# Optimization experiments

Hardware: AMD Instinct MI355X
Metric: run time of the kernel (lower is better)

The kernel has to match this reference:

```python
import jax, jax.numpy as jnp
import numpy as np

NUME = 100000
H, DH, K, R = 4, 32, 16, 17
DIN, DT, DOUT = 128, 32, 128
N0, N1, N2 = 131072, 32768, 4096
B, HIST = 2048, 2
LN_EPS = 1e-5


def setup_inputs() -> dict:
    key = jax.random.key(0)
    ks = jax.random.split(key, 16)
    din = DIN + DT
    inp = {}
    inp["emb"] = jax.random.normal(ks[0], (NUME, DIN), jnp.float32) * 0.1
    inp["freq"] = jnp.asarray(1.0 / 10 ** np.linspace(0, 9, DT), jnp.float32)
    inp["phase"] = jnp.zeros((DT,), jnp.float32)
    for l in (0, 1):
        inp[f"gamma{l}"] = jnp.ones((din,), jnp.float32)
        inp[f"beta{l}"] = jnp.zeros((din,), jnp.float32)
        inp[f"W{l}"] = jax.random.normal(ks[1 + 5 * l], (R, din, H * DH), jnp.float32) * 0.05
        inp[f"attn_l{l}"] = jax.random.normal(ks[2 + 5 * l], (R, H, DH), jnp.float32) * 0.05
        inp[f"attn_r{l}"] = jax.random.normal(ks[3 + 5 * l], (R, H, DH), jnp.float32) * 0.05
        inp[f"bias{l}"] = jnp.zeros((R, H * DH), jnp.float32)
    inp["src_ids0"] = jax.random.randint(ks[11], (N0,), 0, NUME * 100)
    inp["src_idx0"] = jax.random.randint(ks[12], (R, N1, K), 0, N0)
    inp["src_ids1"] = jax.random.randint(ks[13], (N1,), 0, NUME * 100)
    inp["src_idx1"] = jax.random.randint(ks[14], (R, N2, K), 0, N1)
    inp["root_idx"] = jax.random.randint(ks[15], (B * HIST,), 0, N2)
    inp["ts"] = 99
    return inp


def _gat_layer(h, src_ids, src_idx, gamma, beta, W, al, ar, b, ts, freq, phase):
    # h: [Nsrc, din-DT] src-node features; src_idx: [R, Ndst, K] neighbor ids.
    ndst = src_idx.shape[1]
    # TimeEnc: cos((ts - nid // nume) * freq + phase)
    t = (ts - src_ids // NUME).astype(h.dtype)
    phi = jnp.cos(t[:, None] * freq + phase)  # [Nsrc, DT]
    h = jnp.concatenate([h, phi], axis=1)
    # LayerNorm
    mu = jnp.mean(h, axis=-1, keepdims=True)
    var = jnp.mean((h - mu) ** 2, axis=-1, keepdims=True)
    h = (h - mu) * jax.lax.rsqrt(var + LN_EPS) * gamma + beta

    def body(acc, xs):
        Wr, alr, arr, br, idx = xs
        proj = (h @ Wr).reshape(-1, H, DH)               # [Nsrc, H, DH]
        el = jnp.einsum('nhe,he->nh', proj, alr)         # [Nsrc, H]
        er = jnp.einsum('nhe,he->nh', proj[:ndst], arr)  # [Ndst, H]
        e = jax.nn.leaky_relu(el[idx] + er[:, None, :], 0.2)  # [Ndst, K, H]
        a = jax.nn.softmax(e, axis=1)                    # edge softmax over K
        out = jnp.einsum('ikh,ikhe->ihe', a, proj[idx]) + br.reshape(H, DH)
        return acc + out, None

    acc, _ = jax.lax.scan(body, jnp.zeros((ndst, H, DH), h.dtype),
                          (W, al, ar, b, src_idx))
    # HeteroGraphConv aggregate='mean' over R relation outputs, then ReLU
    return jax.nn.relu((acc / R).reshape(ndst, H * DH))


def reference(emb, freq, phase,
              gamma0, beta0, W0, attn_l0, attn_r0, bias0,
              gamma1, beta1, W1, attn_l1, attn_r1, bias1,
              src_ids0, src_idx0, src_ids1, src_idx1, root_idx, ts):
    h = emb[src_ids0 % NUME]  # entity embedding lookup [N0, DIN]
    h = _gat_layer(h, src_ids0, src_idx0, gamma0, beta0, W0, attn_l0, attn_r0,
                   bias0, ts, freq, phase)
    h = _gat_layer(h, src_ids1, src_idx1, gamma1, beta1, W1, attn_l1, attn_r1,
                   bias1, ts, freq, phase)
    # gather root embeddings and fold hist dimension into features
    return h[root_idx].reshape(B, HIST * DOUT)
```

## Files before the change

kernel.cpp:

```cpp
#include <hip/hip_runtime.h>
#include <hip/hip_bf16.h>

#define NUME 100000
constexpr int H      = 4;
constexpr int DH     = 32;
constexpr int KNB    = 16;
constexpr int R      = 17;
constexpr int DIN    = 128;
constexpr int DT     = 32;
constexpr int DINT   = 160;
constexpr int N0     = 131072;
constexpr int N1     = 32768;
constexpr int N2     = 4096;
constexpr float LN_EPS = 1e-5f;

typedef unsigned short ushort_t;
typedef ushort_t us2 __attribute__((ext_vector_type(2)));
typedef ushort_t us8 __attribute__((ext_vector_type(8)));
typedef short    s8v __attribute__((ext_vector_type(8)));
typedef float    f32x4 __attribute__((ext_vector_type(4)));

__device__ __forceinline__ float bf2f(ushort_t u) {
    return __uint_as_float(((unsigned int)u) << 16);
}
__device__ __forceinline__ ushort_t f2bf(float f) {
    unsigned int x = __float_as_uint(f);
    unsigned int r = x + 0x7fffu + ((x >> 16) & 1u);
    return (ushort_t)(r >> 16);
}

__global__ __launch_bounds__(256) void k_wcast(
    const float* __restrict__ W, ushort_t* __restrict__ wt, int total)
{
    int t = blockIdx.x * blockDim.x + threadIdx.x;
    if (t >= total) return;
    int r   = t / (DINT * DIN);
    int rem = t % (DINT * DIN);
    int k   = rem >> 7;
    int n   = rem & 127;
    wt[(size_t)r * DIN * DINT + (size_t)n * DINT + k] = f2bf(W[t]);
}

__global__ __launch_bounds__(256) void k_prep(
    const float* __restrict__ srcf,
    const int*   __restrict__ ids,
    const int*   __restrict__ ts_ptr,
    const float* __restrict__ freq,
    const float* __restrict__ phase,
    const float* __restrict__ gamma,
    const float* __restrict__ beta,
    ushort_t*    __restrict__ hn,
    int n_rows, int mode)
{
    int wid  = (int)((blockIdx.x * blockDim.x + threadIdx.x) >> 6);
    int lane = threadIdx.x & 63;
    if (wid >= n_rows) return;

    int id = ids[wid];
    const float* row = (mode == 1)
        ? (srcf + (size_t)(id % NUME) * DIN)
        : (srcf + (size_t)wid * DIN);

    float x0 = row[lane];
    float x1 = row[lane + 64];
    if (mode == 0) {
        x0 = fmaxf(x0 * (1.f / (float)R), 0.f);
        x1 = fmaxf(x1 * (1.f / (float)R), 0.f);
    }

    int   ts = ts_ptr[0];
    float t  = (float)(ts - id / NUME);
    float p  = 0.f;
    if (lane < DT) p = cosf(t * freq[lane] + phase[lane]);

    float s  = x0 + x1 + p;
    float sq = x0*x0 + x1*x1 + p*p;
    #pragma unroll
    for (int m = 1; m < 64; m <<= 1) {
        s  += __shfl_xor(s,  m);
        sq += __shfl_xor(sq, m);
    }
    float mu   = s / (float)DINT;
    float var  = sq / (float)DINT - mu * mu;
    float rstd = rsqrtf(var + LN_EPS);

    size_t base = (size_t)wid * DINT;
    hn[base + lane]      = f2bf((x0 - mu) * rstd * gamma[lane]      + beta[lane]);
    hn[base + 64 + lane] = f2bf((x1 - mu) * rstd * gamma[64 + lane] + beta[64 + lane]);
    if (lane < DT)
        hn[base + 128 + lane] = f2bf((p - mu) * rstd * gamma[128 + lane] + beta[128 + lane]);
}

__global__ __launch_bounds__(256) void k_gemm(
    const ushort_t* __restrict__ A,
    const ushort_t* __restrict__ Bt,
    const float*    __restrict__ al,
    const float*    __restrict__ ar,
    ushort_t*       __restrict__ C,
    float*          __restrict__ el,
    float*          __restrict__ er,
    int ndst)
{
    __shared__ ushort_t Bs[128][168];
    __shared__ ushort_t As[2][128][40];

    int tid  = threadIdx.x;
    int lane = tid & 63;
    int wave = tid >> 6;
    int wr   = wave >> 1;
    int wc   = wave & 1;
    int row0 = blockIdx.x * 128;

    {
        int bm  = tid >> 1;
        int bko = (tid & 1) * 80;
        #pragma unroll
        for (int g = 0; g < 10; ++g)
            *(us8*)&Bs[bm][bko + g * 8] =
                *(const us8*)&Bt[(size_t)bm * DINT + bko + g * 8];
        #pragma unroll
        for (int j = 0; j < 2; ++j) {
            int f  = tid + j * 256;
            int m  = f >> 2;
            int ko = (f & 3) * 8;
            *(us8*)&As[0][m][ko] = *(const us8*)&A[(size_t)(row0 + m) * DINT + ko];
        }
    }
    __syncthreads();

    s8v breg[5][4];
    #pragma unroll
    for (int kk = 0; kk < 5; ++kk)
        #pragma unroll
        for (int j = 0; j < 4; ++j)
            breg[kk][j] = *(const s8v*)&Bs[wc*64 + j*16 + (lane & 15)]
                                          [kk*32 + (lane >> 4) * 8];

    f32x4 acc[4][4];
    #pragma unroll
    for (int i = 0; i < 4; ++i)
        #pragma unroll
        for (int j = 0; j < 4; ++j) acc[i][j] = (f32x4){0.f, 0.f, 0.f, 0.f};

    #pragma unroll
    for (int kc = 0; kc < 5; ++kc) {
        us8 pa[2];
        int m0 = 0, ko0 = 0, m1 = 0, ko1 = 0;
        if (kc < 4) {
            int f0 = tid;
            m0  = f0 >> 2; ko0 = (f0 & 3) * 8;
            pa[0] = *(const us8*)&A[(size_t)(row0 + m0) * DINT + (kc + 1) * 32 + ko0];
            int f1 = tid + 256;
            m1  = f1 >> 2; ko1 = (f1 & 3) * 8;
            pa[1] = *(const us8*)&A[(size_t)(row0 + m1) * DINT + (kc + 1) * 32 + ko1];
        }

        s8v af[4];
        #pragma unroll
        for (int i = 0; i < 4; ++i)
            af[i] = *(const s8v*)&As[kc & 1][wr*64 + i*16 + (lane & 15)]
                                            [(lane >> 4) * 8];
        #pragma unroll
        for (int i = 0; i < 4; ++i)
            #pragma unroll
            for (int j = 0; j < 4; ++j)
                acc[i][j] = __builtin_amdgcn_mfma_f32_16x16x32_bf16(
                                af[i], breg[kc][j], acc[i][j], 0, 0, 0);

        if (kc < 4) {
            *(us8*)&As[(kc + 1) & 1][m0][ko0] = pa[0];
            *(us8*)&As[(kc + 1) & 1][m1][ko1] = pa[1];
        }
        __syncthreads();
    }

    #pragma unroll
    for (int i = 0; i < 4; ++i) {
        #pragma unroll
        for (int j = 0; j < 4; ++j) {
            int col  = wc*64 + j*16 + (lane & 15);
            int rowb = row0 + wr*64 + i*16 + ((lane >> 4) << 2);
            #pragma unroll
            for (int q = 0; q < 4; ++q)
                C[(size_t)(rowb + q) * DIN + col] = f2bf(acc[i][j][q]);
        }
    }

    float alv[4], arv[4];
    #pragma unroll
    for (int j = 0; j < 4; ++j) {
        int c = wc*64 + j*16 + (lane & 15);
        alv[j] = al[c];
        arv[j] = ar[c];
    }
    int b0 = lane & 1;
    int b1 = (lane >> 1) & 1;
    #pragma unroll
    for (int i = 0; i < 4; ++i) {
        #pragma unroll
        for (int q = 0; q < 4; ++q) {
            float pl0 = acc[i][0][q]*alv[0] + acc[i][1][q]*alv[1];
            float pl1 = acc[i][2][q]*alv[2] + acc[i][3][q]*alv[3];
            float pr0 = acc[i][0][q]*arv[0] + acc[i][1][q]*arv[1];
            float pr1 = acc[i][2][q]*arv[2] + acc[i][3][q]*arv[3];
            float t;
            t = __shfl_xor(b0 ? pl0 : pl1, 1);
            float vA = (b0 ? pl1 : pl0) + t;
            t = __shfl_xor(b0 ? pr0 : pr1, 1);
            float vB = (b0 ? pr1 : pr0) + t;
            t = __shfl_xor(b1 ? vA : vB, 2);
            float vC = (b1 ? vB : vA) + t;
            vC += __shfl_xor(vC, 4);
            vC += __shfl_xor(vC, 8);
            if ((lane & 12) == 0) {
                int row = row0 + wr*64 + i*16 + ((lane >> 4) << 2) + q;
                int h   = 2*wc + b0;
                if (!b1) {
                    el[(size_t)row * 4 + h] = vC;
                } else if (row < ndst) {
                    er[(size_t)row * 4 + h] = vC;
                }
            }
        }
    }
}

__global__ __launch_bounds__(256) void k_agg(
    const ushort_t* __restrict__ proj,
    const int*      __restrict__ idx,
    const float*    __restrict__ el,
    const float*    __restrict__ er,
    const float*    __restrict__ br,
    float*          __restrict__ accg,
    int ndst)
{
    int wid  = (int)((blockIdx.x * blockDim.x + threadIdx.x) >> 6);
    if (wid >= ndst) return;
    int l = threadIdx.x & 63;

    int jv = idx[(size_t)wid * KNB + (l & 15)];

    int   jk = __shfl(jv, l >> 2);
    float e  = el[(size_t)jk * 4 + (l & 3)] + er[(size_t)wid * 4 + (l & 3)];
    e = e > 0.f ? e : 0.2f * e;
    float mx = e;
    #pragma unroll
    for (int m = 4; m < 64; m <<= 1) mx = fmaxf(mx, __shfl_xor(mx, m));
    float p = __expf(e - mx);
    float s = p;
    #pragma unroll
    for (int m = 4; m < 64; m <<= 1) s += __shfl_xor(s, m);
    float a = p / s;

    int rsub = l >> 4;
    int fg   = l & 15;
    float vacc[8];
    #pragma unroll
    for (int t = 0; t < 8; ++t) vacc[t] = 0.f;

    #pragma unroll
    for (int kk = 0; kk < 4; ++kk) {
        int   j  = __shfl(jv, 4*kk + rsub);
        float ak = __shfl(a, 16*kk + 4*rsub + (fg >> 2));
        us8   v  = *(const us8*)&proj[(size_t)j * DIN + fg * 8];
        #pragma unroll
        for (int t = 0; t < 8; ++t) vacc[t] = fmaf(ak, bf2f(v[t]), vacc[t]);
    }
    #pragma unroll
    for (int t = 0; t < 8; ++t) {
        vacc[t] += __shfl_xor(vacc[t], 16);
        vacc[t] += __shfl_xor(vacc[t], 32);
    }
    if (l < 16) {
        float* ap = accg + (size_t)wid * DIN + l * 8;
        #pragma unroll
        for (int t = 0; t < 8; ++t) ap[t] += vacc[t] + br[l * 8 + t];
    }
}

__global__ __launch_bounds__(256) void k_root(
    const float* __restrict__ acc, const int* __restrict__ root,
    float* __restrict__ out, int n)
{
    int t = blockIdx.x * blockDim.x + threadIdx.x;
    if (t < n) {
        float x = acc[(size_t)root[t >> 7] * DIN + (t & 127)];
        out[t] = fmaxf(x * (1.f / (float)R), 0.f);
    }
}

extern "C" void kernel_launch(void* const* d_in, const int* in_sizes, int n_in,
                              void* d_out, int out_size, void* d_ws, size_t ws_size,
                              hipStream_t stream)
{
    const float* emb    = (const float*)d_in[0];
    const float* freq   = (const float*)d_in[1];
    const float* phase  = (const float*)d_in[2];
    const float* gamma0 = (const float*)d_in[3];
    const float* beta0  = (const float*)d_in[4];
    const float* W0     = (const float*)d_in[5];
    const float* al0    = (const float*)d_in[6];
    const float* ar0    = (const float*)d_in[7];
    const float* b0     = (const float*)d_in[8];
    const float* gamma1 = (const float*)d_in[9];
    const float* beta1  = (const float*)d_in[10];
    const float* W1     = (const float*)d_in[11];
    const float* al1    = (const float*)d_in[12];
    const float* ar1    = (const float*)d_in[13];
    const float* b1     = (const float*)d_in[14];
    const int* src_ids0 = (const int*)d_in[15];
    const int* src_idx0 = (const int*)d_in[16];
    const int* src_ids1 = (const int*)d_in[17];
    const int* src_idx1 = (const int*)d_in[18];
    const int* root     = (const int*)d_in[19];
    const int* ts       = (const int*)d_in[20];
    float* out = (float*)d_out;

    ushort_t* hn   = (ushort_t*)d_ws;
    ushort_t* proj = hn   + (size_t)N0 * DINT;
    float*    acc  = (float*)(proj + (size_t)N0 * DIN);
    float*    el   = acc  + (size_t)N1 * DIN;
    float*    er   = el   + (size_t)N0 * 4;
    ushort_t* wt0  = (ushort_t*)(er + (size_t)N1 * 4);
    ushort_t* wt1  = wt0 + (size_t)R * DIN * DINT;

    const int WTOT = R * DINT * DIN;

    k_wcast<<<(WTOT + 255) / 256, 256, 0, stream>>>(W0, wt0, WTOT);
    hipMemsetAsync(acc, 0, (size_t)N1 * DIN * sizeof(float), stream);
    k_prep<<<N0 / 4, 256, 0, stream>>>(emb, src_ids0, ts, freq, phase,
                                       gamma0, beta0, hn, N0, 1);
    for (int r = 0; r < R; ++r) {
        k_gemm<<<N0 / 128, 256, 0, stream>>>(hn, wt0 + (size_t)r * DIN * DINT,
                                             al0 + r * 128, ar0 + r * 128,
                                             proj, el, er, N1);
        k_agg<<<N1 / 4, 256, 0, stream>>>(proj,
                                          src_idx0 + (size_t)r * N1 * KNB,
                                          el, er, b0 + r * 128, acc, N1);
    }

    k_wcast<<<(WTOT + 255) / 256, 256, 0, stream>>>(W1, wt1, WTOT);
    k_prep<<<N1 / 4, 256, 0, stream>>>(acc, src_ids1, ts, freq, phase,
                                       gamma1, beta1, hn, N1, 0);
    hipMemsetAsync(acc, 0, (size_t)N2 * DIN * sizeof(float), stream);
    for (int r = 0; r < R; ++r) {
        k_gemm<<<N1 / 128, 256, 0, stream>>>(hn, wt1 + (size_t)r * DIN * DINT,
                                             al1 + r * 128, ar1 + r * 128,
                                             proj, el, er, N2);
        k_agg<<<N2 / 4, 256, 0, stream>>>(proj,
                                          src_idx1 + (size_t)r * N2 * KNB,
                                          el, er, b1 + r * 128, acc, N2);
    }

    k_root<<<(N2 * DIN) / 256, 256, 0, stream>>>(acc, root, out, N2 * DIN);
}
```

Baseline: 1.447 ms.

## Batch layer-1 relations into one GEMM and fused aggregation, hoist bias sums

Layer 1 now runs one GEMM launch over all 17 relations via blockIdx.y, storing per-relation projections, followed by a single aggregation kernel. That kernel loops over relations in registers and writes acc once, which removes 34 launches and the repeated read-modify-write of acc. Per-relation biases are pre-summed once and folded into the next prep step or the root kernel instead of being added on every aggregation. Prep handles two rows per wave with float4 loads, and the aggregation kernel issues its neighbor loads before the softmax to hide latency. The batched path needs extra workspace and falls back to the old loop when ws_size is too small.

Measured after the change: 1.208 ms. -16.6%, faster.

```diff
diff --git a/kernel.cpp b/kernel.cpp
--- a/kernel.cpp
+++ b/kernel.cpp
@@ -15,7 +15,7 @@
 constexpr float LN_EPS = 1e-5f;
 
 typedef unsigned short ushort_t;
-typedef ushort_t us2 __attribute__((ext_vector_type(2)));
+typedef ushort_t us4 __attribute__((ext_vector_type(4)));
 typedef ushort_t us8 __attribute__((ext_vector_type(8)));
 typedef short    s8v __attribute__((ext_vector_type(8)));
 typedef float    f32x4 __attribute__((ext_vector_type(4)));
@@ -39,6 +39,19 @@
     int k   = rem >> 7;
     int n   = rem & 127;
     wt[(size_t)r * DIN * DINT + (size_t)n * DINT + k] = f2bf(W[t]);
+}
+
+__global__ __launch_bounds__(256) void k_bsum(
+    const float* __restrict__ b0, const float* __restrict__ b1,
+    float* __restrict__ bsum01)
+{
+    int t = threadIdx.x;
+    const float* b = (t < 128) ? b0 : b1;
+    int c = t & 127;
+    float s = 0.f;
+    #pragma unroll
+    for (int r = 0; r < R; ++r) s += b[r * 128 + c];
+    bsum01[t] = s;
 }
 
 __global__ __launch_bounds__(256) void k_prep(
@@ -49,34 +62,39 @@
     const float* __restrict__ phase,
     const float* __restrict__ gamma,
     const float* __restrict__ beta,
+    const float* __restrict__ bsum,
     ushort_t*    __restrict__ hn,
     int n_rows, int mode)
 {
-    int wid  = (int)((blockIdx.x * blockDim.x + threadIdx.x) >> 6);
+    int wv   = (int)((blockIdx.x * blockDim.x + threadIdx.x) >> 6);
     int lane = threadIdx.x & 63;
-    if (wid >= n_rows) return;
-
-    int id = ids[wid];
-    const float* row = (mode == 1)
+    int half = lane >> 5;
+    int l5   = lane & 31;
+    int row  = wv * 2 + half;
+    if (row >= n_rows) return;
+
+    int id = ids[row];
+    const float* rp = (mode == 1)
         ? (srcf + (size_t)(id % NUME) * DIN)
-        : (srcf + (size_t)wid * DIN);
-
-    float x0 = row[lane];
-    float x1 = row[lane + 64];
+        : (srcf + (size_t)row * DIN);
+
+    float4 x = *(const float4*)&rp[l5 * 4];
     if (mode == 0) {
-        x0 = fmaxf(x0 * (1.f / (float)R), 0.f);
-        x1 = fmaxf(x1 * (1.f / (float)R), 0.f);
+        const float4 bs = *(const float4*)&bsum[l5 * 4];
+        x.x = fmaxf((x.x + bs.x) * (1.f / (float)R), 0.f);
+        x.y = fmaxf((x.y + bs.y) * (1.f / (float)R), 0.f);
+        x.z = fmaxf((x.z + bs.z) * (1.f / (float)R), 0.f);
+        x.w = fmaxf((x.w + bs.w) * (1.f / (float)R), 0.f);
     }
 
     int   ts = ts_ptr[0];
     float t  = (float)(ts - id / NUME);
-    float p  = 0.f;
-    if (lane < DT) p = cosf(t * freq[lane] + phase[lane]);
-
-    float s  = x0 + x1 + p;
-    float sq = x0*x0 + x1*x1 + p*p;
-    #pragma unroll
-    for (int m = 1; m < 64; m <<= 1) {
+    float p  = cosf(t * freq[l5] + phase[l5]);
+
+    float s  = x.x + x.y + x.z + x.w + p;
+    float sq = x.x*x.x + x.y*x.y + x.z*x.z + x.w*x.w + p*p;
+    #pragma unroll
+    for (int m = 1; m < 32; m <<= 1) {
         s  += __shfl_xor(s,  m);
         sq += __shfl_xor(sq, m);
     }
@@ -84,25 +102,36 @@
     float var  = sq / (float)DINT - mu * mu;
     float rstd = rsqrtf(var + LN_EPS);
 
-    size_t base = (size_t)wid * DINT;
-    hn[base + lane]      = f2bf((x0 - mu) * rstd * gamma[lane]      + beta[lane]);
-    hn[base + 64 + lane] = f2bf((x1 - mu) * rstd * gamma[64 + lane] + beta[64 + lane]);
-    if (lane < DT)
-        hn[base + 128 + lane] = f2bf((p - mu) * rstd * gamma[128 + lane] + beta[128 + lane]);
+    size_t base = (size_t)row * DINT;
+    us4 pk;
+    pk[0] = f2bf((x.x - mu) * rstd * gamma[l5*4+0] + beta[l5*4+0]);
+    pk[1] = f2bf((x.y - mu) * rstd * gamma[l5*4+1] + beta[l5*4+1]);
+    pk[2] = f2bf((x.z - mu) * rstd * gamma[l5*4+2] + beta[l5*4+2]);
+    pk[3] = f2bf((x.w - mu) * rstd * gamma[l5*4+3] + beta[l5*4+3]);
+    *(us4*)&hn[base + l5*4] = pk;
+    hn[base + 128 + l5] = f2bf((p - mu) * rstd * gamma[128 + l5] + beta[128 + l5]);
 }
 
 __global__ __launch_bounds__(256) void k_gemm(
     const ushort_t* __restrict__ A,
-    const ushort_t* __restrict__ Bt,
-    const float*    __restrict__ al,
-    const float*    __restrict__ ar,
-    ushort_t*       __restrict__ C,
-    float*          __restrict__ el,
-    float*          __restrict__ er,
-    int ndst)
+    const ushort_t* __restrict__ BtB,
+    const float*    __restrict__ alB,
+    const float*    __restrict__ arB,
+    ushort_t*       __restrict__ CB,
+    float*          __restrict__ elB,
+    float*          __restrict__ erB,
+    int ndst, int M)
 {
     __shared__ ushort_t Bs[128][168];
     __shared__ ushort_t As[2][128][40];
+
+    int r = blockIdx.y;
+    const ushort_t* Bt = BtB + (size_t)r * DIN * DINT;
+    const float*    al = alB + (size_t)r * DIN;
+    const float*    ar = arB + (size_t)r * DIN;
+    ushort_t*       C  = CB  + (size_t)r * M * DIN;
+    float*          el = elB + (size_t)r * M * 4;
+    float*          er = erB + (size_t)r * ndst * 4;
 
     int tid  = threadIdx.x;
     int lane = tid & 63;
@@ -225,20 +254,29 @@
     }
 }
 
-__global__ __launch_bounds__(256) void k_agg(
+__global__ __launch_bounds__(256) void k_agg_r(
     const ushort_t* __restrict__ proj,
     const int*      __restrict__ idx,
     const float*    __restrict__ el,
     const float*    __restrict__ er,
-    const float*    __restrict__ br,
     float*          __restrict__ accg,
     int ndst)
 {
     int wid  = (int)((blockIdx.x * blockDim.x + threadIdx.x) >> 6);
     if (wid >= ndst) return;
-    int l = threadIdx.x & 63;
+    int l    = threadIdx.x & 63;
+    int rsub = l >> 4;
+    int fg   = l & 15;
 
     int jv = idx[(size_t)wid * KNB + (l & 15)];
+
+    int j2[4];
+    us8 v[4];
+    #pragma unroll
+    for (int kk = 0; kk < 4; ++kk) j2[kk] = __shfl(jv, 4*kk + rsub);
+    #pragma unroll
+    for (int kk = 0; kk < 4; ++kk)
+        v[kk] = *(const us8*)&proj[(size_t)j2[kk] * DIN + fg * 8];
 
     int   jk = __shfl(jv, l >> 2);
     float e  = el[(size_t)jk * 4 + (l & 3)] + er[(size_t)wid * 4 + (l & 3)];
@@ -252,19 +290,14 @@
     for (int m = 4; m < 64; m <<= 1) s += __shfl_xor(s, m);
     float a = p / s;
 
-    int rsub = l >> 4;
-    int fg   = l & 15;
     float vacc[8];
     #pragma unroll
     for (int t = 0; t < 8; ++t) vacc[t] = 0.f;
-
     #pragma unroll
     for (int kk = 0; kk < 4; ++kk) {
-        int   j  = __shfl(jv, 4*kk + rsub);
         float ak = __shfl(a, 16*kk + 4*rsub + (fg >> 2));
-        us8   v  = *(const us8*)&proj[(size_t)j * DIN + fg * 8];
-        #pragma unroll
-        for (int t = 0; t < 8; ++t) vacc[t] = fmaf(ak, bf2f(v[t]), vacc[t]);
+        #pragma unroll
+        for (int t = 0; t < 8; ++t) vacc[t] = fmaf(ak, bf2f(v[kk][t]), vacc[t]);
     }
     #pragma unroll
     for (int t = 0; t < 8; ++t) {
@@ -274,17 +307,83 @@
     if (l < 16) {
         float* ap = accg + (size_t)wid * DIN + l * 8;
         #pragma unroll
-        for (int t = 0; t < 8; ++t) ap[t] += vacc[t] + br[l * 8 + t];
+        for (int t = 0; t < 8; ++t) ap[t] += vacc[t];
+    }
+}
+
+__global__ __launch_bounds__(256) void k_agg_all(
+    const ushort_t* __restrict__ projB,
+    const int*      __restrict__ idxB,
+    const float*    __restrict__ elB,
+    const float*    __restrict__ erB,
+    float*          __restrict__ accg,
+    int ndst, int nsrc)
+{
+    int wid  = (int)((blockIdx.x * blockDim.x + threadIdx.x) >> 6);
+    if (wid >= ndst) return;
+    int l    = threadIdx.x & 63;
+    int rsub = l >> 4;
+    int fg   = l & 15;
+
+    float vacc[8];
+    #pragma unroll
+    for (int t = 0; t < 8; ++t) vacc[t] = 0.f;
+
+    for (int r = 0; r < R; ++r) {
+        const ushort_t* proj = projB + (size_t)r * nsrc * DIN;
+        const int*      idx  = idxB  + (size_t)r * ndst * KNB;
+        const float*    el   = elB   + (size_t)r * nsrc * 4;
+        const float*    er   = erB   + (size_t)r * ndst * 4;
+
+        int jv = idx[(size_t)wid * KNB + (l & 15)];
+
+        int j2[4];
+        us8 v[4];
+        #pragma unroll
+        for (int kk = 0; kk < 4; ++kk) j2[kk] = __shfl(jv, 4*kk + rsub);
+        #pragma unroll
+        for (int kk = 0; kk < 4; ++kk)
+            v[kk] = *(const us8*)&proj[(size_t)j2[kk] * DIN + fg * 8];
+
+        int   jk = __shfl(jv, l >> 2);
+        float e  = el[(size_t)jk * 4 + (l & 3)] + er[(size_t)wid * 4 + (l & 3)];
+        e = e > 0.f ? e : 0.2f * e;
+        float mx = e;
+        #pragma unroll
+        for (int m = 4; m < 64; m <<= 1) mx = fmaxf(mx, __shfl_xor(mx, m));
+        float p = __expf(e - mx);
+        float s = p;
+        #pragma unroll
+        for (int m = 4; m < 64; m <<= 1) s += __shfl_xor(s, m);
+        float a = p / s;
+
+        #pragma unroll
+        for (int kk = 0; kk < 4; ++kk) {
+            float ak = __shfl(a, 16*kk + 4*rsub + (fg >> 2));
+            #pragma unroll
+            for (int t = 0; t < 8; ++t) vacc[t] = fmaf(ak, bf2f(v[kk][t]), vacc[t]);
+        }
+    }
+
+    #pragma unroll
+    for (int t = 0; t < 8; ++t) {
+        vacc[t] += __shfl_xor(vacc[t], 16);
+        vacc[t] += __shfl_xor(vacc[t], 32);
+    }
+    if (l < 16) {
+        float* ap = accg + (size_t)wid * DIN + l * 8;
+        #pragma unroll
+        for (int t = 0; t < 8; ++t) ap[t] = vacc[t];
     }
 }
 
 __global__ __launch_bounds__(256) void k_root(
     const float* __restrict__ acc, const int* __restrict__ root,
-    float* __restrict__ out, int n)
+    const float* __restrict__ bsum1, float* __restrict__ out, int n)
 {
     int t = blockIdx.x * blockDim.x + threadIdx.x;
     if (t < n) {
-        float x = acc[(size_t)root[t >> 7] * DIN + (t & 127)];
+        float x = acc[(size_t)root[t >> 7] * DIN + (t & 127)] + bsum1[t & 127];
         out[t] = fmaxf(x * (1.f / (float)R), 0.f);
     }
 }
@@ -316,41 +415,62 @@
     const int* ts       = (const int*)d_in[20];
     float* out = (float*)d_out;
 
-    ushort_t* hn   = (ushort_t*)d_ws;
-    ushort_t* proj = hn   + (size_t)N0 * DINT;
-    float*    acc  = (float*)(proj + (size_t)N0 * DIN);
-    float*    el   = acc  + (size_t)N1 * DIN;
-    float*    er   = el   + (size_t)N0 * 4;
-    ushort_t* wt0  = (ushort_t*)(er + (size_t)N1 * 4);
-    ushort_t* wt1  = wt0 + (size_t)R * DIN * DINT;
+    char* cur = (char*)d_ws;
+    auto carve = [&](size_t bytes) {
+        char* p = cur;
+        cur += (bytes + 255) & ~(size_t)255;
+        return (void*)p;
+    };
+    ushort_t* hn    = (ushort_t*)carve((size_t)N0 * DINT * 2);
+    float*    acc   = (float*)carve((size_t)N1 * DIN * 4);
+    ushort_t* wt0   = (ushort_t*)carve((size_t)R * DIN * DINT * 2);
+    ushort_t* wt1   = (ushort_t*)carve((size_t)R * DIN * DINT * 2);
+    float*    bsum  = (float*)carve(256 * 4);
+    ushort_t* proj  = (ushort_t*)carve((size_t)N0 * DIN * 2);
+    float*    el0   = (float*)carve((size_t)N0 * 4 * 4);
+    float*    er0   = (float*)carve((size_t)N1 * 4 * 4);
+    size_t baseC = (size_t)(cur - (char*)d_ws);
+    ushort_t* proj1 = (ushort_t*)carve((size_t)R * N1 * DIN * 2);
+    float*    el1   = (float*)carve((size_t)R * N1 * 4 * 4);
+    float*    er1   = (float*)carve((size_t)R * N2 * 4 * 4);
+    size_t needB = (size_t)(cur - (char*)d_ws);
+    const bool batchedL1 = (ws_size >= needB);
+    (void)baseC;
 
     const int WTOT = R * DINT * DIN;
 
+    k_bsum<<<1, 256, 0, stream>>>(b0, b1, bsum);
     k_wcast<<<(WTOT + 255) / 256, 256, 0, stream>>>(W0, wt0, WTOT);
+    k_wcast<<<(WTOT + 255) / 256, 256, 0, stream>>>(W1, wt1, WTOT);
+
     hipMemsetAsync(acc, 0, (size_t)N1 * DIN * sizeof(float), stream);
-    k_prep<<<N0 / 4, 256, 0, stream>>>(emb, src_ids0, ts, freq, phase,
-                                       gamma0, beta0, hn, N0, 1);
+    k_prep<<<N0 / 8, 256, 0, stream>>>(emb, src_ids0, ts, freq, phase,
+                                       gamma0, beta0, bsum, hn, N0, 1);
     for (int r = 0; r < R; ++r) {
-        k_gemm<<<N0 / 128, 256, 0, stream>>>(hn, wt0 + (size_t)r * DIN * DINT,
-                                             al0 + r * 128, ar0 + r * 128,
-                                             proj, el, er, N1);
-        k_agg<<<N1 / 4, 256, 0, stream>>>(proj,
-                                          src_idx0 + (size_t)r * N1 * KNB,
-                                          el, er, b0 + r * 128, acc, N1);
-    }
-
-    k_wcast<<<(WTOT + 255) / 256, 256, 0, stream>>>(W1, wt1, WTOT);
-    k_prep<<<N1 / 4, 256, 0, stream>>>(acc, src_ids1, ts, freq, phase,
-                                       gamma1, beta1, hn, N1, 0);
-    hipMemsetAsync(acc, 0, (size_t)N2 * DIN * sizeof(float), stream);
-    for (int r = 0; r < R; ++r) {
-        k_gemm<<<N1 / 128, 256, 0, stream>>>(hn, wt1 + (size_t)r * DIN * DINT,
-                                             al1 + r * 128, ar1 + r * 128,
-                                             proj, el, er, N2);
-        k_agg<<<N2 / 4, 256, 0, stream>>>(proj,
-                                          src_idx1 + (size_t)r * N2 * KNB,
-                                          el, er, b1 + r * 128, acc, N2);
-    }
-
-    k_root<<<(N2 * DIN) / 256, 256, 0, stream>>>(acc, root, out, N2 * DIN);
-}
+        k_gemm<<<dim3(N0 / 128, 1), 256, 0, stream>>>(
+            hn, wt0 + (size_t)r * DIN * DINT, al0 + r * 128, ar0 + r * 128,
+            proj, el0, er0, N1, N0);
+        k_agg_r<<<N1 / 4, 256, 0, stream>>>(
+            proj, src_idx0 + (size_t)r * N1 * KNB, el0, er0, acc, N1);
+    }
+
+    k_prep<<<N1 / 8, 256, 0, stream>>>(acc, src_ids1, ts, freq, phase,
+                                       gamma1, beta1, bsum, hn, N1, 0);
+    if (batchedL1) {
+        k_gemm<<<dim3(N1 / 128, R), 256, 0, stream>>>(
+            hn, wt1, al1, ar1, proj1, el1, er1, N2, N1);
+        k_agg_all<<<N2 / 4, 256, 0, stream>>>(
+            proj1, src_idx1, el1, er1, acc, N2, N1);
+    } else {
+        hipMemsetAsync(acc, 0, (size_t)N2 * DIN * sizeof(float), stream);
+        for (int r = 0; r < R; ++r) {
+            k_gemm<<<dim3(N1 / 128, 1), 256, 0, stream>>>(
+                hn, wt1 + (size_t)r * DIN * DINT, al1 + r * 128, ar1 + r * 128,
+                proj, el0, er0, N2, N1);
+            k_agg_r<<<N2 / 4, 256, 0, stream>>>(
+                proj, src_idx1 + (size_t)r * N2 * KNB, el0, er0, acc, N2);
+        }
+    }
+
+    k_root<<<(N2 * DIN) / 256, 256, 0, stream>>>(acc, root, bsum + 128, out, N2 * DIN);
+}
```
